# Optimization experiments

Hardware: AMD Instinct MI355X
Metric: run time of the kernel (lower is better)

The kernel has to match this reference:

```python
import jax, jax.numpy as jnp
import numpy as np

D = 1024
H = 16
DH = D // H
B = 8
T = 1024
EPS = 1e-5


def setup_inputs() -> dict:
    key = jax.random.key(0)
    ks = jax.random.split(key, 12)
    s = 0.02
    return {
        "x": jax.random.normal(ks[0], (B, T, D), dtype=jnp.float32),
        "ln1_scale": jnp.ones((D,), jnp.float32),
        "ln1_shift": jnp.zeros((D,), jnp.float32),
        "Wq": jax.random.normal(ks[1], (D, D), jnp.float32) * s,
        "Wk": jax.random.normal(ks[2], (D, D), jnp.float32) * s,
        "Wv": jax.random.normal(ks[3], (D, D), jnp.float32) * s,
        "Wo": jax.random.normal(ks[4], (D, D), jnp.float32) * s,
        "bo": jnp.zeros((D,), jnp.float32),
        "ln2_scale": jnp.ones((D,), jnp.float32),
        "ln2_shift": jnp.zeros((D,), jnp.float32),
        "W1": jax.random.normal(ks[5], (D, 4 * D), jnp.float32) * s,
        "b1": jnp.zeros((4 * D,), jnp.float32),
        "W2": jax.random.normal(ks[6], (4 * D, D), jnp.float32) * s,
        "b2": jnp.zeros((D,), jnp.float32),
    }


def _layernorm(x, scale, shift):
    mean = jnp.mean(x, axis=-1, keepdims=True)
    var = jnp.mean((x - mean) ** 2, axis=-1, keepdims=True)  # unbiased=False
    return (x - mean) * jax.lax.rsqrt(var + EPS) * scale + shift


def _gelu_tanh(x):
    c = jnp.sqrt(jnp.float32(2.0 / jnp.pi))
    return 0.5 * x * (1.0 + jnp.tanh(c * (x + 0.044715 * x ** 3)))


def reference(x, ln1_scale, ln1_shift, Wq, Wk, Wv, Wo, bo,
              ln2_scale, ln2_shift, W1, b1, W2, b2):
    b, t, d = x.shape
    x1 = _layernorm(x, ln1_scale, ln1_shift)
    # QKV projections (no bias), split heads -> (b, h, t, d_h)
    q = (x1 @ Wq).reshape(b, t, H, DH).transpose(0, 2, 1, 3)
    k = (x1 @ Wk).reshape(b, t, H, DH).transpose(0, 2, 1, 3)
    v = (x1 @ Wv).reshape(b, t, H, DH).transpose(0, 2, 1, 3)
    scores = jnp.einsum("bhqd,bhkd->bhqk", q, k) / jnp.sqrt(jnp.float32(DH))
    # original does tril then adds -inf upper-triangular mask -> standard causal mask
    causal = jnp.tril(jnp.ones((t, t), dtype=bool))
    scores = jnp.where(causal, scores, -jnp.inf)
    attn = jax.nn.softmax(scores, axis=-1)
    z = jnp.einsum("bhqk,bhkd->bhqd", attn, v)
    z = z.transpose(0, 2, 1, 3).reshape(b, t, d)
    x2 = z @ Wo + bo
    y = x2 + x
    y1 = _layernorm(y, ln2_scale, ln2_shift)
    y2 = _gelu_tanh(y1 @ W1 + b1) @ W2 + b2
    return y2 + y
```

## Files before the change

kernel.cpp:

```cpp
#include <hip/hip_runtime.h>

typedef unsigned short u16;
typedef __bf16 bf16x8 __attribute__((ext_vector_type(8)));
typedef float f32x4 __attribute__((ext_vector_type(4)));

#define D_MODEL 1024
#define NHEAD 16
#define DHEAD 64
#define BATCH 8
#define SEQ 1024
#define NROW 8192

__device__ __forceinline__ u16 f2bf(float f) {
  union { float f; unsigned int u; } a; a.f = f;
  unsigned int u = a.u;
  return (u16)((u + 0x7fffu + ((u >> 16) & 1u)) >> 16);
}

__device__ __forceinline__ float bf2f(u16 b) {
  union { unsigned int u; float f; } a; a.u = ((unsigned int)b) << 16;
  return a.f;
}

__device__ __forceinline__ float gelu_f(float x) {
  float y = 0.79788456080286535588f * (x + 0.044715f * x * x * x);
  return x / (1.0f + __expf(-2.0f * y));
}

__device__ __forceinline__ void async16(const void* gsrc, void* ldst) {
  __builtin_amdgcn_global_load_lds((__attribute__((address_space(1))) void*)gsrc,
                                   (__attribute__((address_space(3))) void*)ldst,
                                   16, 0, 0);
}

__global__ __launch_bounds__(256)
void wconv_kernel(const float* __restrict__ W, u16* __restrict__ WT, int K, int N) {
  __shared__ float tile[32][33];
  const int tx = threadIdx.x & 31, ty = threadIdx.x >> 5;
  const int n0 = blockIdx.x * 32, k0 = blockIdx.y * 32;
#pragma unroll
  for (int r = 0; r < 4; ++r)
    tile[ty + r * 8][tx] = W[(size_t)(k0 + ty + r * 8) * N + n0 + tx];
  __syncthreads();
#pragma unroll
  for (int r = 0; r < 4; ++r)
    WT[(size_t)(n0 + ty + r * 8) * K + k0 + tx] = f2bf(tile[tx][ty + r * 8]);
}

__global__ __launch_bounds__(256)
void ln_kernel(const float* __restrict__ x, const float* __restrict__ gamma,
               const float* __restrict__ beta, u16* __restrict__ out) {
  const int row = blockIdx.x, t = threadIdx.x;
  const float4 v = ((const float4*)(x + (size_t)row * D_MODEL))[t];
  float s  = v.x + v.y + v.z + v.w;
  float s2 = v.x * v.x + v.y * v.y + v.z * v.z + v.w * v.w;
#pragma unroll
  for (int off = 32; off >= 1; off >>= 1) {
    s  += __shfl_down(s, off);
    s2 += __shfl_down(s2, off);
  }
  __shared__ float red[8];
  const int w = t >> 6, l = t & 63;
  if (l == 0) { red[w] = s; red[4 + w] = s2; }
  __syncthreads();
  s  = red[0] + red[1] + red[2] + red[3];
  s2 = red[4] + red[5] + red[6] + red[7];
  const float mean = s * (1.0f / D_MODEL);
  const float var  = s2 * (1.0f / D_MODEL) - mean * mean;
  const float inv  = rsqrtf(var + 1e-5f);
  const float4 ga = ((const float4*)gamma)[t];
  const float4 be = ((const float4*)beta)[t];
  ushort4 ov;
  ov.x = f2bf((v.x - mean) * inv * ga.x + be.x);
  ov.y = f2bf((v.y - mean) * inv * ga.y + be.y);
  ov.z = f2bf((v.z - mean) * inv * ga.z + be.z);
  ov.w = f2bf((v.w - mean) * inv * ga.w + be.w);
  ((ushort4*)out)[(size_t)row * 256 + t] = ov;
}

__global__ __launch_bounds__(256)
void ln_bf16_kernel(const u16* __restrict__ x, const float* __restrict__ gamma,
                    const float* __restrict__ beta, u16* __restrict__ out) {
  const int row = blockIdx.x, t = threadIdx.x;
  const ushort4 bv = ((const ushort4*)(x + (size_t)row * D_MODEL))[t];
  float4 v;
  v.x = bf2f(bv.x); v.y = bf2f(bv.y); v.z = bf2f(bv.z); v.w = bf2f(bv.w);
  float s  = v.x + v.y + v.z + v.w;
  float s2 = v.x * v.x + v.y * v.y + v.z * v.z + v.w * v.w;
#pragma unroll
  for (int off = 32; off >= 1; off >>= 1) {
    s  += __shfl_down(s, off);
    s2 += __shfl_down(s2, off);
  }
  __shared__ float red[8];
  const int w = t >> 6, l = t & 63;
  if (l == 0) { red[w] = s; red[4 + w] = s2; }
  __syncthreads();
  s  = red[0] + red[1] + red[2] + red[3];
  s2 = red[4] + red[5] + red[6] + red[7];
  const float mean = s * (1.0f / D_MODEL);
  const float var  = s2 * (1.0f / D_MODEL) - mean * mean;
  const float inv  = rsqrtf(var + 1e-5f);
  const float4 ga = ((const float4*)gamma)[t];
  const float4 be = ((const float4*)beta)[t];
  ushort4 ov;
  ov.x = f2bf((v.x - mean) * inv * ga.x + be.x);
  ov.y = f2bf((v.y - mean) * inv * ga.y + be.y);
  ov.z = f2bf((v.z - mean) * inv * ga.z + be.z);
  ov.w = f2bf((v.w - mean) * inv * ga.w + be.w);
  ((ushort4*)out)[(size_t)row * 256 + t] = ov;
}

#define MODE_QK 0
#define MODE_VT 1
#define MODE_YRES 2
#define MODE_GELU 3
#define MODE_OUT 4

template <int MODE>
__global__ __launch_bounds__(256, 4)
void gemm_bt(const u16* __restrict__ A, const u16* __restrict__ BT,
             const float* __restrict__ bias, const float* __restrict__ resid,
             void* __restrict__ outp, int M, int N, int K) {
  __shared__ u16 sA[2][128 * 32];
  __shared__ u16 sB[2][128 * 32];
  const int t = threadIdx.x;
  const int w = t >> 6, l = t & 63;
  const int c = l & 15, g = l >> 4;
  const int wr = w >> 1, wc = w & 1;
  const int bm = blockIdx.x, bn = blockIdx.y;

  f32x4 acc[4][4] = {};

  const char* Ab = (const char*)(A + (size_t)bm * 128 * K);
  const char* Bb = (const char*)(BT + (size_t)bn * 128 * K);
  const size_t ldb = (size_t)K * 2;
  const int srow = t >> 2;
  const int scolb = (t & 3) * 16;
  const int ldsoff = w * 1024;

  auto stage = [&](int buf, int k0) {
#pragma unroll
    for (int i = 0; i < 2; ++i) {
      async16(Ab + (size_t)(srow + i * 64) * ldb + (size_t)k0 * 2 + scolb,
              (char*)sA[buf] + i * 4096 + ldsoff);
      async16(Bb + (size_t)(srow + i * 64) * ldb + (size_t)k0 * 2 + scolb,
              (char*)sB[buf] + i * 4096 + ldsoff);
    }
  };

  stage(0, 0);
  asm volatile("s_waitcnt vmcnt(0)" ::: "memory");
  __builtin_amdgcn_s_barrier();

  const int nt = K >> 5;
  for (int it = 0; it < nt; ++it) {
    const int cur = it & 1;
    if (it + 1 < nt) stage(cur ^ 1, (it + 1) << 5);
    bf16x8 af[4], bfr[4];
#pragma unroll
    for (int m = 0; m < 4; ++m)
      af[m] = *(const bf16x8*)&sA[cur][(wr * 64 + m * 16 + c) * 32 + g * 8];
#pragma unroll
    for (int n = 0; n < 4; ++n)
      bfr[n] = *(const bf16x8*)&sB[cur][(wc * 64 + n * 16 + c) * 32 + g * 8];
#pragma unroll
    for (int m = 0; m < 4; ++m)
#pragma unroll
      for (int n = 0; n < 4; ++n)
        acc[m][n] = __builtin_amdgcn_mfma_f32_16x16x32_bf16(af[m], bfr[n], acc[m][n], 0, 0, 0);
    asm volatile("s_waitcnt vmcnt(0)" ::: "memory");
    __builtin_amdgcn_s_barrier();
  }

#pragma unroll
  for (int m = 0; m < 4; ++m) {
    const int r0 = bm * 128 + wr * 64 + m * 16 + g * 4;
#pragma unroll
    for (int n = 0; n < 4; ++n) {
      const int cc = bn * 128 + wc * 64 + n * 16 + c;
#pragma unroll
      for (int i = 0; i < 4; ++i) {
        const int r = r0 + i;
        const float v = acc[m][n][i];
        if constexpr (MODE == MODE_QK) {
          ((u16*)outp)[(((size_t)(r >> 10) * NHEAD + (cc >> 6)) * SEQ + (r & 1023)) * DHEAD + (cc & 63)] = f2bf(v);
        } else if constexpr (MODE == MODE_VT) {
          ((u16*)outp)[(((size_t)(r >> 10) * NHEAD + (cc >> 6)) * DHEAD + (cc & 63)) * SEQ + (r & 1023)] = f2bf(v);
        } else if constexpr (MODE == MODE_YRES) {
          const size_t idx = (size_t)r * N + cc;
          ((u16*)outp)[idx] = f2bf(v + bias[cc] + resid[idx]);
        } else if constexpr (MODE == MODE_OUT) {
          const size_t idx = (size_t)r * N + cc;
          ((float*)outp)[idx] = v + bias[cc] + bf2f(((const u16*)resid)[idx]);
        } else {
          const size_t idx = (size_t)r * N + cc;
          ((u16*)outp)[idx] = f2bf(gelu_f(v + bias[cc]));
        }
      }
    }
  }
}

__global__ __launch_bounds__(256, 3)
void attn_kernel(const u16* __restrict__ q, const u16* __restrict__ k,
                 const u16* __restrict__ vT, u16* __restrict__ z) {
  __shared__ u16 sK[2][64 * 64];
  __shared__ u16 sV[2][64 * 64];
  __shared__ u16 pb[4][32 * 64];

  const int t = threadIdx.x, w = t >> 6, l = t & 63;
  const int c = l & 15, g = l >> 4;
  const int bh = blockIdx.y;
  const int qb0 = blockIdx.x * 128;
  const int qw0 = qb0 + w * 32;

  const u16* qbase = q  + (size_t)bh * SEQ * DHEAD;
  const u16* kbase = k  + (size_t)bh * SEQ * DHEAD;
  const u16* vbase = vT + (size_t)bh * DHEAD * SEQ;

  bf16x8 qf[2][2];
#pragma unroll
  for (int j = 0; j < 2; ++j)
#pragma unroll
    for (int hh = 0; hh < 2; ++hh)
      qf[j][hh] = *(const bf16x8*)&qbase[(size_t)(qw0 + j * 16 + c) * DHEAD + hh * 32 + g * 8];

  f32x4 o[4][2] = {};
  float m[2]  = {-3.0e38f, -3.0e38f};
  float ls[2] = {0.0f, 0.0f};

  const int r8 = l >> 3, ch = l & 7;
  const int sw16 = (ch ^ r8) * 16;

  auto stage = [&](int buf, int kt) {
    const int kb0 = kt * 64;
#pragma unroll
    for (int i = 0; i < 2; ++i) {
      const int row = w * 8 + i * 32 + r8;
      async16((const char*)kbase + (size_t)(kb0 + row) * 128 + sw16,
              (char*)sK[buf] + w * 1024 + i * 4096);
      async16((const char*)vbase + (size_t)row * (SEQ * 2) + (size_t)kb0 * 2 + sw16,
              (char*)sV[buf] + w * 1024 + i * 4096);
    }
  };

  const int nkt = blockIdx.x * 2 + 2;
  stage(0, 0);

  for (int kt = 0; kt < nkt; ++kt) {
    const int cur = kt & 1;
    if (kt + 1 < nkt) {
      stage(cur ^ 1, kt + 1);
      asm volatile("s_waitcnt vmcnt(4)" ::: "memory");
    } else {
      asm volatile("s_waitcnt vmcnt(0)" ::: "memory");
    }
    __builtin_amdgcn_s_barrier();

    const int kb0 = kt * 64;
    if (kb0 < qw0 + 32) {
      const u16* sKc = sK[cur];
      const u16* sVc = sV[cur];
      const int cx = c & 7;

      f32x4 st[4][2];
#pragma unroll
      for (int s = 0; s < 4; ++s) {
        const int row = s * 16 + c;
        bf16x8 kf0 = *(const bf16x8*)&sKc[row * 64 + ((0 + g) ^ cx) * 8];
        bf16x8 kf1 = *(const bf16x8*)&sKc[row * 64 + ((4 + g) ^ cx) * 8];
#pragma unroll
        for (int j = 0; j < 2; ++j) {
          f32x4 z4 = {};
          z4 = __builtin_amdgcn_mfma_f32_16x16x32_bf16(kf0, qf[j][0], z4, 0, 0, 0);
          z4 = __builtin_amdgcn_mfma_f32_16x16x32_bf16(kf1, qf[j][1], z4, 0, 0, 0);
          st[s][j] = z4;
        }
      }

      const bool full = (kb0 + 64 <= qw0 + 1);
      float tmax[2] = {-3.0e38f, -3.0e38f};
#pragma unroll
      for (int s = 0; s < 4; ++s)
#pragma unroll
        for (int j = 0; j < 2; ++j)
#pragma unroll
          for (int i = 0; i < 4; ++i) {
            float vsc = st[s][j][i] * 0.125f;
            if (!full) {
              const int key = kb0 + s * 16 + g * 4 + i;
              vsc = (key <= qw0 + j * 16 + c) ? vsc : -1.0e30f;
            }
            st[s][j][i] = vsc;
            tmax[j] = fmaxf(tmax[j], vsc);
          }
#pragma unroll
      for (int j = 0; j < 2; ++j) {
        tmax[j] = fmaxf(tmax[j], __shfl_xor(tmax[j], 16));
        tmax[j] = fmaxf(tmax[j], __shfl_xor(tmax[j], 32));
      }
      float mnew[2], sc[2], psum[2];
#pragma unroll
      for (int j = 0; j < 2; ++j) {
        mnew[j] = fmaxf(m[j], tmax[j]);
        sc[j]   = __expf(m[j] - mnew[j]);
        psum[j] = 0.0f;
      }
#pragma unroll
      for (int s = 0; s < 4; ++s)
#pragma unroll
        for (int j = 0; j < 2; ++j)
#pragma unroll
          for (int i = 0; i < 4; ++i) {
            const float pv = __expf(st[s][j][i] - mnew[j]);
            st[s][j][i] = pv;
            psum[j] += pv;
          }
#pragma unroll
      for (int j = 0; j < 2; ++j) {
        psum[j] += __shfl_xor(psum[j], 16);
        psum[j] += __shfl_xor(psum[j], 32);
        ls[j] = ls[j] * sc[j] + psum[j];
        m[j]  = mnew[j];
#pragma unroll
        for (int d = 0; d < 4; ++d) o[d][j] = o[d][j] * sc[j];
      }

      u16* pw = pb[w];
#pragma unroll
      for (int s = 0; s < 4; ++s)
#pragma unroll
        for (int j = 0; j < 2; ++j) {
          const int row = j * 16 + c;
          const int swz = (s * 2 + (g >> 1)) ^ cx;
          ushort4 pv4;
          pv4.x = f2bf(st[s][j][0]); pv4.y = f2bf(st[s][j][1]);
          pv4.z = f2bf(st[s][j][2]); pv4.w = f2bf(st[s][j][3]);
          *(ushort4*)&pw[row * 64 + swz * 8 + (g & 1) * 4] = pv4;
        }

      bf16x8 pf[2][2];
#pragma unroll
      for (int j = 0; j < 2; ++j)
#pragma unroll
        for (int ks = 0; ks < 2; ++ks)
          pf[j][ks] = *(const bf16x8*)&pw[(j * 16 + c) * 64 + ((ks * 4 + g) ^ cx) * 8];

#pragma unroll
      for (int d = 0; d < 4; ++d) {
        const int vrow = d * 16 + c;
#pragma unroll
        for (int ks = 0; ks < 2; ++ks) {
          bf16x8 vf = *(const bf16x8*)&sVc[vrow * 64 + ((ks * 4 + g) ^ cx) * 8];
#pragma unroll
          for (int j = 0; j < 2; ++j)
            o[d][j] = __builtin_amdgcn_mfma_f32_16x16x32_bf16(vf, pf[j][ks], o[d][j], 0, 0, 0);
        }
      }
    }
    __builtin_amdgcn_s_barrier();
  }

  const int b = bh >> 4, h = bh & 15;
#pragma unroll
  for (int j = 0; j < 2; ++j) {
    const float inv = 1.0f / ls[j];
    const int qrow = qw0 + j * 16 + c;
    u16* zr = z + ((size_t)b * SEQ + qrow) * D_MODEL + h * DHEAD;
#pragma unroll
    for (int d = 0; d < 4; ++d) {
      ushort4 ov;
      ov.x = f2bf(o[d][j][0] * inv); ov.y = f2bf(o[d][j][1] * inv);
      ov.z = f2bf(o[d][j][2] * inv); ov.w = f2bf(o[d][j][3] * inv);
      *(ushort4*)&zr[d * 16 + g * 4] = ov;
    }
  }
}

extern "C" void kernel_launch(void* const* d_in, const int* in_sizes, int n_in,
                              void* d_out, int out_size, void* d_ws, size_t ws_size,
                              hipStream_t stream) {
  (void)in_sizes; (void)n_in; (void)out_size; (void)ws_size;
  const float* x   = (const float*)d_in[0];
  const float* g1  = (const float*)d_in[1];
  const float* s1  = (const float*)d_in[2];
  const float* Wq  = (const float*)d_in[3];
  const float* Wk  = (const float*)d_in[4];
  const float* Wv  = (const float*)d_in[5];
  const float* Wo  = (const float*)d_in[6];
  const float* bo  = (const float*)d_in[7];
  const float* g2  = (const float*)d_in[8];
  const float* s2  = (const float*)d_in[9];
  const float* W1  = (const float*)d_in[10];
  const float* b1  = (const float*)d_in[11];
  const float* W2  = (const float*)d_in[12];
  const float* b2  = (const float*)d_in[13];
  float* out = (float*)d_out;
  char* ws = (char*)d_ws;
  const size_t MB = 1024 * 1024;

  u16* wqT = (u16*)(ws + 0 * MB);
  u16* wkT = (u16*)(ws + 2 * MB);
  u16* wvT = (u16*)(ws + 4 * MB);
  u16* woT = (u16*)(ws + 6 * MB);
  u16* w1T = (u16*)(ws + 8 * MB);
  u16* w2T = (u16*)(ws + 16 * MB);
  u16* x1  = (u16*)(ws + 24 * MB);
  u16* qb  = (u16*)(ws + 40 * MB);
  u16* kb  = (u16*)(ws + 56 * MB);
  u16* vb  = (u16*)(ws + 72 * MB);
  u16* hb  = (u16*)(ws + 24 * MB);
  u16* zb  = (u16*)(ws + 88 * MB);
  u16* y1  = (u16*)(ws + 88 * MB);
  u16* yb  = (u16*)(ws + 104 * MB);

  wconv_kernel<<<dim3(32, 32), 256, 0, stream>>>(Wq, wqT, 1024, 1024);
  wconv_kernel<<<dim3(32, 32), 256, 0, stream>>>(Wk, wkT, 1024, 1024);
  wconv_kernel<<<dim3(32, 32), 256, 0, stream>>>(Wv, wvT, 1024, 1024);
  wconv_kernel<<<dim3(32, 32), 256, 0, stream>>>(Wo, woT, 1024, 1024);
  wconv_kernel<<<dim3(128, 32), 256, 0, stream>>>(W1, w1T, 1024, 4096);
  wconv_kernel<<<dim3(32, 128), 256, 0, stream>>>(W2, w2T, 4096, 1024);
  ln_kernel<<<NROW, 256, 0, stream>>>(x, g1, s1, x1);
  gemm_bt<MODE_QK><<<dim3(64, 8), 256, 0, stream>>>(x1, wqT, nullptr, nullptr, qb, NROW, 1024, 1024);
  gemm_bt<MODE_QK><<<dim3(64, 8), 256, 0, stream>>>(x1, wkT, nullptr, nullptr, kb, NROW, 1024, 1024);
  gemm_bt<MODE_VT><<<dim3(64, 8), 256, 0, stream>>>(x1, wvT, nullptr, nullptr, vb, NROW, 1024, 1024);
  attn_kernel<<<dim3(8, 128), 256, 0, stream>>>(qb, kb, vb, zb);
  gemm_bt<MODE_YRES><<<dim3(64, 8), 256, 0, stream>>>(zb, woT, bo, x, yb, NROW, 1024, 1024);
  ln_bf16_kernel<<<NROW, 256, 0, stream>>>(yb, g2, s2, y1);
  gemm_bt<MODE_GELU><<<dim3(64, 32), 256, 0, stream>>>(y1, w1T, b1, nullptr,
                                                       hb, NROW, 4096, 1024);
  gemm_bt<MODE_OUT><<<dim3(64, 8), 256, 0, stream>>>(hb, w2T, b2, (const float*)yb,
                                                     out, NROW, 1024, 4096);
}
```

Measured before the change: 398.2 us.

## Triple-buffer GEMM K-loop with partial vmcnt waits and batch square weight conversions

Adds an NBUF template parameter to the bf16 GEMM. With three LDS buffers, each iteration waits only until the oldest stage has landed (vmcnt(4)), then issues the load two tiles ahead before computing, so global-to-LDS copies overlap MFMA work better. The triple-buffered path is used for all GEMMs except the wide GELU one, which keeps double buffering. Separately, the four 1024x1024 weight transposes become a single launch using blockIdx.z. The extra buffer raises LDS per block from 32KB to 48KB, which may reduce occupancy.

```diff
diff --git a/kernel.cpp b/kernel.cpp
--- a/kernel.cpp
+++ b/kernel.cpp
@@ -31,6 +31,30 @@
   __builtin_amdgcn_global_load_lds((__attribute__((address_space(1))) void*)gsrc,
                                    (__attribute__((address_space(3))) void*)ldst,
                                    16, 0, 0);
+}
+
+template <int N> __device__ __forceinline__ void vmwait() {
+  if constexpr (N == 4)      asm volatile("s_waitcnt vmcnt(4)" ::: "memory");
+  else                       asm volatile("s_waitcnt vmcnt(0)" ::: "memory");
+}
+
+__global__ __launch_bounds__(256)
+void wconv4_kernel(const float* __restrict__ Wa, const float* __restrict__ Wb,
+                   const float* __restrict__ Wc, const float* __restrict__ Wd,
+                   u16* __restrict__ WT) {
+  const float* Ws[4] = {Wa, Wb, Wc, Wd};
+  const float* W = Ws[blockIdx.z];
+  u16* dst = WT + (size_t)blockIdx.z * 1024 * 1024;
+  __shared__ float tile[32][33];
+  const int tx = threadIdx.x & 31, ty = threadIdx.x >> 5;
+  const int n0 = blockIdx.x * 32, k0 = blockIdx.y * 32;
+#pragma unroll
+  for (int r = 0; r < 4; ++r)
+    tile[ty + r * 8][tx] = W[(size_t)(k0 + ty + r * 8) * 1024 + n0 + tx];
+  __syncthreads();
+#pragma unroll
+  for (int r = 0; r < 4; ++r)
+    dst[(size_t)(n0 + ty + r * 8) * 1024 + k0 + tx] = f2bf(tile[tx][ty + r * 8]);
 }
 
 __global__ __launch_bounds__(256)
@@ -117,13 +141,13 @@
 #define MODE_GELU 3
 #define MODE_OUT 4
 
-template <int MODE>
+template <int MODE, int NBUF>
 __global__ __launch_bounds__(256, 4)
 void gemm_bt(const u16* __restrict__ A, const u16* __restrict__ BT,
              const float* __restrict__ bias, const float* __restrict__ resid,
              void* __restrict__ outp, int M, int N, int K) {
-  __shared__ u16 sA[2][128 * 32];
-  __shared__ u16 sB[2][128 * 32];
+  __shared__ u16 sA[NBUF][128 * 32];
+  __shared__ u16 sB[NBUF][128 * 32];
   const int t = threadIdx.x;
   const int w = t >> 6, l = t & 63;
   const int c = l & 15, g = l >> 4;
@@ -149,14 +173,7 @@
     }
   };
 
-  stage(0, 0);
-  asm volatile("s_waitcnt vmcnt(0)" ::: "memory");
-  __builtin_amdgcn_s_barrier();
-
-  const int nt = K >> 5;
-  for (int it = 0; it < nt; ++it) {
-    const int cur = it & 1;
-    if (it + 1 < nt) stage(cur ^ 1, (it + 1) << 5);
+  auto compute = [&](int cur) {
     bf16x8 af[4], bfr[4];
 #pragma unroll
     for (int m = 0; m < 4; ++m)
@@ -169,8 +186,31 @@
 #pragma unroll
       for (int n = 0; n < 4; ++n)
         acc[m][n] = __builtin_amdgcn_mfma_f32_16x16x32_bf16(af[m], bfr[n], acc[m][n], 0, 0, 0);
-    asm volatile("s_waitcnt vmcnt(0)" ::: "memory");
+  };
+
+  const int nt = K >> 5;
+
+  if constexpr (NBUF == 2) {
+    stage(0, 0);
+    vmwait<0>();
     __builtin_amdgcn_s_barrier();
+    for (int it = 0; it < nt; ++it) {
+      const int cur = it & 1;
+      if (it + 1 < nt) stage(cur ^ 1, (it + 1) << 5);
+      compute(cur);
+      vmwait<0>();
+      __builtin_amdgcn_s_barrier();
+    }
+  } else {
+    stage(0, 0);
+    stage(1, 32);
+    for (int it = 0; it < nt; ++it) {
+      const int cur = it % 3;
+      if (it + 1 < nt) vmwait<4>(); else vmwait<0>();
+      __builtin_amdgcn_s_barrier();
+      if (it + 2 < nt) stage((it + 2) % 3, (it + 2) << 5);
+      compute(cur);
+    }
   }
 
 #pragma unroll
@@ -415,21 +455,18 @@
   u16* y1  = (u16*)(ws + 88 * MB);
   u16* yb  = (u16*)(ws + 104 * MB);
 
-  wconv_kernel<<<dim3(32, 32), 256, 0, stream>>>(Wq, wqT, 1024, 1024);
-  wconv_kernel<<<dim3(32, 32), 256, 0, stream>>>(Wk, wkT, 1024, 1024);
-  wconv_kernel<<<dim3(32, 32), 256, 0, stream>>>(Wv, wvT, 1024, 1024);
-  wconv_kernel<<<dim3(32, 32), 256, 0, stream>>>(Wo, woT, 1024, 1024);
+  wconv4_kernel<<<dim3(32, 32, 4), 256, 0, stream>>>(Wq, Wk, Wv, Wo, wqT);
   wconv_kernel<<<dim3(128, 32), 256, 0, stream>>>(W1, w1T, 1024, 4096);
   wconv_kernel<<<dim3(32, 128), 256, 0, stream>>>(W2, w2T, 4096, 1024);
   ln_kernel<<<NROW, 256, 0, stream>>>(x, g1, s1, x1);
-  gemm_bt<MODE_QK><<<dim3(64, 8), 256, 0, stream>>>(x1, wqT, nullptr, nullptr, qb, NROW, 1024, 1024);
-  gemm_bt<MODE_QK><<<dim3(64, 8), 256, 0, stream>>>(x1, wkT, nullptr, nullptr, kb, NROW, 1024, 1024);
-  gemm_bt<MODE_VT><<<dim3(64, 8), 256, 0, stream>>>(x1, wvT, nullptr, nullptr, vb, NROW, 1024, 1024);
+  gemm_bt<MODE_QK, 3><<<dim3(64, 8), 256, 0, stream>>>(x1, wqT, nullptr, nullptr, qb, NROW, 1024, 1024);
+  gemm_bt<MODE_QK, 3><<<dim3(64, 8), 256, 0, stream>>>(x1, wkT, nullptr, nullptr, kb, NROW, 1024, 1024);
+  gemm_bt<MODE_VT, 3><<<dim3(64, 8), 256, 0, stream>>>(x1, wvT, nullptr, nullptr, vb, NROW, 1024, 1024);
   attn_kernel<<<dim3(8, 128), 256, 0, stream>>>(qb, kb, vb, zb);
-  gemm_bt<MODE_YRES><<<dim3(64, 8), 256, 0, stream>>>(zb, woT, bo, x, yb, NROW, 1024, 1024);
+  gemm_bt<MODE_YRES, 3><<<dim3(64, 8), 256, 0, stream>>>(zb, woT, bo, x, yb, NROW, 1024, 1024);
   ln_bf16_kernel<<<NROW, 256, 0, stream>>>(yb, g2, s2, y1);
-  gemm_bt<MODE_GELU><<<dim3(64, 32), 256, 0, stream>>>(y1, w1T, b1, nullptr,
-                                                       hb, NROW, 4096, 1024);
-  gemm_bt<MODE_OUT><<<dim3(64, 8), 256, 0, stream>>>(hb, w2T, b2, (const float*)yb,
-                                                     out, NROW, 1024, 4096);
-}
+  gemm_bt<MODE_GELU, 2><<<dim3(64, 32), 256, 0, stream>>>(y1, w1T, b1, nullptr,
+                                                          hb, NROW, 4096, 1024);
+  gemm_bt<MODE_OUT, 3><<<dim3(64, 8), 256, 0, stream>>>(hb, w2T, b2, (const float*)yb,
+                                                        out, NROW, 1024, 4096);
+}
```

Result: no change. 403.5 us (+1.3%).
